# Kernel tuning notes

Hardware: AMD Instinct MI355X
Metric: run time of the kernel (lower is better)

The kernel has to match this reference:

```python
import jax, jax.numpy as jnp
import numpy as np

N_E = 1024
E_DIM = 256
BETA = 0.25
EPS = 1e-10


def setup_inputs() -> dict:
    key = jax.random.key(0)
    k1, k2 = jax.random.split(key)
    z = jax.random.normal(k1, (32, E_DIM, 32, 32), dtype=jnp.float32)
    emb = jax.random.normal(k2, (N_E, E_DIM), dtype=jnp.float32)
    return {"z": z, "emb": emb}


def reference(z, emb):
    sg = jax.lax.stop_gradient
    # (B, C, H, W) -> (B, H, W, C)
    zp = jnp.transpose(z, (0, 2, 3, 1))
    zf = zp.reshape(-1, E_DIM)  # (N, C), N = B*H*W
    # squared euclidean distances: ||z||^2 + ||e||^2 - 2 z e^T  -> (N, n_e)
    d = (jnp.sum(zf * zf, axis=1, keepdims=True)
         + jnp.sum(emb * emb, axis=1)
         - 2.0 * jnp.matmul(zf, emb.T))
    idx = jnp.argmin(d, axis=1)  # (N,)
    # one-hot @ codebook == gather (same math, no dense one-hot matmul)
    z_q1 = emb[idx].reshape(zp.shape)  # (B, H, W, C)
    # loss: note original does NOT detach z_q1 anywhere
    loss = jnp.mean((z_q1 - zp) ** 2) + BETA * jnp.mean((z_q1 - sg(zp)) ** 2)
    # straight-through (original detaches z, not z_q1)
    z_q = zp + (z_q1 - sg(zp))
    # perplexity from mean one-hot encodings = normalized histogram of indices
    counts = jnp.bincount(idx, length=N_E)
    e_mean = counts.astype(zf.dtype) / idx.shape[0]
    perplexity = jnp.exp(-jnp.sum(e_mean * jnp.log(e_mean + EPS)))
    z_q = jnp.transpose(z_q, (0, 3, 1, 2))
    z_q1_out = jnp.transpose(z_q1, (0, 3, 1, 2))
    return loss, z_q, perplexity, idx, z_q1_out
```

## Files before the change

### kernel.cpp

```cpp
#include <hip/hip_runtime.h>
#include <hip/hip_bf16.h>
#include <math.h>

#define CDIM 256
#define HW   1024
#define NVEC 32768
#define NE   1024
#define ZSIZE 8388608
#define NSPLIT 4
#define MARGIN 0.12f
#define ZPCAP 15360

#define OUT_LOSS 0
#define OUT_ZQ   1
#define OUT_PERP 8388609
#define OUT_IDX  8388610
#define OUT_ZQ1  8421378

#define WS_LOSS   0
#define WS_RCNT   64
#define WS_HIST   128
#define WS_ENORM  4224
#define WS_IDX    8448
#define WS_RLIST  139520
#define WS_S1     270592
#define WS_S2     794880
#define WS_J1     1319168
#define WS_SCORE  1843456
#define WS_EBH    2105600
#define WS_ZBH    2629888
#define WS_ZPACK  19407104

typedef __attribute__((ext_vector_type(8))) short short8;
typedef __attribute__((ext_vector_type(4))) float f32x4;
typedef __attribute__((ext_vector_type(8))) unsigned short ushort8v;
typedef __attribute__((ext_vector_type(8))) _Float16 half8;

__device__ __forceinline__ unsigned short f16_rne(float x) {
    _Float16 h = (_Float16)x;
    return __builtin_bit_cast(unsigned short, h);
}
__device__ __forceinline__ void lds_barrier() {
    asm volatile("s_waitcnt lgkmcnt(0)\n\ts_barrier" ::: "memory");
}

__global__ __launch_bounds__(256) void vq_prep(
    const float* __restrict__ z, const float* __restrict__ emb,
    unsigned short* __restrict__ zbh, unsigned short* __restrict__ ebh,
    float* __restrict__ enorm, int* __restrict__ wsz)
{
    const int tid = threadIdx.x, w = tid >> 6, L = tid & 63;
    if (blockIdx.x < 512) {
        __shared__ unsigned short th[64 * 264];
        const int b = blockIdx.x >> 4, hw0 = (blockIdx.x & 15) << 6;
        const float* zp = z + (size_t)b * (CDIM * HW) + hw0;
        for (int i = 0; i < 16; ++i) {
            int k = (i * 4 + w) * 4;
            float f0 = zp[(size_t)(k + 0) * HW + L];
            float f1 = zp[(size_t)(k + 1) * HW + L];
            float f2 = zp[(size_t)(k + 2) * HW + L];
            float f3 = zp[(size_t)(k + 3) * HW + L];
            ushort4 hi = { f16_rne(f0), f16_rne(f1), f16_rne(f2), f16_rne(f3) };
            *(ushort4*)&th[L * 264 + k] = hi;
        }
        __syncthreads();
#pragma unroll
        for (int it = 0; it < 8; ++it) {
            int row = it * 8 + (tid >> 5);
            int kc = (tid & 31) * 8;
            size_t o = (size_t)(b * 1024 + hw0 + row) * CDIM + kc;
            *(ushort8v*)(zbh + o) = *(ushort8v*)&th[row * 264 + kc];
        }
    } else {
        if (blockIdx.x == 512) {
            for (int i = tid; i < 1056; i += 256) wsz[i] = 0;
        }
        const int cb = (int)(blockIdx.x - 512) * 64;
        for (int p = 0; p < 16; ++p) {
            int code = cb + p * 4 + w;
            float4 v = *(const float4*)(emb + (size_t)code * CDIM + L * 4);
            float s = v.x * v.x + v.y * v.y + v.z * v.z + v.w * v.w;
            for (int off = 32; off; off >>= 1) s += __shfl_down(s, off, 64);
            if (L == 0) enorm[code] = s;
            ushort4 hi = { f16_rne(v.x), f16_rne(v.y), f16_rne(v.z), f16_rne(v.w) };
            *(ushort4*)(ebh + (size_t)code * CDIM + L * 4) = hi;
        }
    }
}

__global__ __launch_bounds__(256, 3) void vq_mfma3(
    const unsigned short* __restrict__ zbh, const unsigned short* __restrict__ ebh,
    const float* __restrict__ enorm,
    float* __restrict__ s1_ws, float* __restrict__ s2_ws, int* __restrict__ j1_ws)
{
    __shared__ short bbuf[2][2048];
    __shared__ float en_s[256];

    const int tid = threadIdx.x, w = tid >> 6, L = tid & 63;
    const int l15 = L & 15, q = L >> 4;
    const int r16 = tid & 15, ch = (tid >> 4) & 3;
    const int mtile = blockIdx.x & 255, js = blockIdx.x >> 8;
    const int n0 = mtile << 7;
    const int jsbase = js << 8;

    half8 AH[2][8];
#pragma unroll
    for (int mf = 0; mf < 2; ++mf)
#pragma unroll
        for (int kk = 0; kk < 8; ++kk)
            AH[mf][kk] = *(const half8*)(zbh + (size_t)(n0 + w * 32 + mf * 16 + l15) * CDIM + kk * 32 + q * 8);

    en_s[tid] = enorm[jsbase + tid];

    float s1[2][4], s2[2][4]; int j1[2][4];
#pragma unroll
    for (int mf = 0; mf < 2; ++mf)
#pragma unroll
        for (int r = 0; r < 4; ++r) { s1[mf][r] = -3.4e38f; s2[mf][r] = -3.4e38f; j1[mf][r] = 0; }

    const unsigned short* ebase = ebh + (size_t)(jsbase + w * 16 + r16) * CDIM + ch * 8;

    short8 st[2];
    st[0] = *(const short8*)(ebase);
    *(short8*)(bbuf[0] + w * 512 + L * 8) = st[0];
    st[1] = *(const short8*)(ebase + 32);
    st[0] = *(const short8*)(ebase + 64);
    lds_barrier();

    f32x4 acc[2][4];
#pragma unroll 8
    for (int t = 0; t < 32; ++t) {
        const int kk = t & 7;
        if (kk == 0) {
#pragma unroll
            for (int mf = 0; mf < 2; ++mf)
#pragma unroll
                for (int jf = 0; jf < 4; ++jf)
                    acc[mf][jf] = (f32x4){0.f, 0.f, 0.f, 0.f};
        }
        const short* bb = bbuf[t & 1];
#pragma unroll
        for (int jf = 0; jf < 4; ++jf) {
            half8 B = *(const half8*)(bb + jf * 512 + L * 8);
            acc[0][jf] = __builtin_amdgcn_mfma_f32_16x16x32_f16(AH[0][kk], B, acc[0][jf], 0, 0, 0);
            acc[1][jf] = __builtin_amdgcn_mfma_f32_16x16x32_f16(AH[1][kk], B, acc[1][jf], 0, 0, 0);
        }
        if (t < 31) {
            *(short8*)(bbuf[(t + 1) & 1] + w * 512 + L * 8) = st[(t + 1) & 1];
            if (t < 29) {
                const int t3 = t + 3;
                st[(t + 1) & 1] = *(const short8*)(ebase + (size_t)(t3 >> 3) * (64 * CDIM) + (t3 & 7) * 32);
            }
            lds_barrier();
        }
        if (kk == 7) {
            const int jg = t >> 3;
#pragma unroll
            for (int jf = 0; jf < 4; ++jf) {
                const int jl = jg * 64 + jf * 16 + l15;
                const int j = jsbase + jl;
                const float hn = 0.5f * en_s[jl];
#pragma unroll
                for (int mf = 0; mf < 2; ++mf)
#pragma unroll
                    for (int r = 0; r < 4; ++r) {
                        float s = acc[mf][jf][r] - hn;
                        if (s > s1[mf][r]) { s2[mf][r] = s1[mf][r]; s1[mf][r] = s; j1[mf][r] = j; }
                        else if (s > s2[mf][r]) s2[mf][r] = s;
                    }
            }
        }
    }

#pragma unroll
    for (int mf = 0; mf < 2; ++mf)
#pragma unroll
        for (int r = 0; r < 4; ++r) {
            float a1 = s1[mf][r], a2 = s2[mf][r]; int aj = j1[mf][r];
            for (int m = 1; m < 16; m <<= 1) {
                float o1 = __shfl_xor(a1, m, 64);
                float o2 = __shfl_xor(a2, m, 64);
                int   oj = __shfl_xor(aj, m, 64);
                if (o1 > a1 || (o1 == a1 && oj < aj)) { a2 = fmaxf(a1, o2); a1 = o1; aj = oj; }
                else a2 = fmaxf(a2, o1);
            }
            if (l15 == 0) {
                int o = js * NVEC + n0 + w * 32 + mf * 16 + q * 4 + r;
                s1_ws[o] = a1; s2_ws[o] = a2; j1_ws[o] = aj;
            }
        }
}

__global__ __launch_bounds__(256) void vq_merge(
    const float* __restrict__ s1_ws, const float* __restrict__ s2_ws,
    const int* __restrict__ j1_ws, int* __restrict__ idx_ws,
    float* __restrict__ idx_out, int* __restrict__ hist,
    int* __restrict__ rcnt, int* __restrict__ rlist,
    unsigned long long* __restrict__ score)
{
    int n = blockIdx.x * 256 + threadIdx.x;
    score[n] = 0ull;
    float b1 = -3.4e38f, b2 = -3.4e38f; int bj = 0;
#pragma unroll
    for (int s = 0; s < NSPLIT; ++s) {
        float a1 = s1_ws[s * NVEC + n], a2 = s2_ws[s * NVEC + n];
        int aj = j1_ws[s * NVEC + n];
        if (a1 > b1 || (a1 == b1 && aj < bj)) { b2 = fmaxf(b1, a2); b1 = a1; bj = aj; }
        else b2 = fmaxf(b2, a1);
    }
    if (b1 - b2 < MARGIN) {
        idx_ws[n] = -1;
        int p = atomicAdd(rcnt, 1); rlist[p] = n;
    } else {
        idx_ws[n] = bj;
        idx_out[n] = (float)bj;
        atomicAdd(&hist[bj], 1);
    }
}

__global__ __launch_bounds__(256) void vq_zpack(
    const float* __restrict__ z, const int* __restrict__ rcnt,
    const int* __restrict__ rlist, float* __restrict__ zpack)
{
    const int count = min(*rcnt, ZPCAP);
    for (int it = blockIdx.x; it < count; it += gridDim.x) {
        const int n = rlist[it];
        zpack[(size_t)it * 256 + threadIdx.x] =
            z[(size_t)(n >> 10) * (CDIM * HW) + (size_t)threadIdx.x * HW + (n & 1023)];
    }
}

__global__ __launch_bounds__(256) void vq_rescue(
    const float* __restrict__ z, const float* __restrict__ emb,
    const float* __restrict__ enorm, const int* __restrict__ rcnt,
    const int* __restrict__ rlist, const float* __restrict__ zpack,
    unsigned long long* __restrict__ score)
{
    __shared__ float en_s[64];
    __shared__ __align__(16) float zrow[256];
    __shared__ float rs[4];
    __shared__ int   rj[4];
    const int tid = threadIdx.x;
    const int wv = tid >> 6, L = tid & 63;
    const int chunk = blockIdx.x & 15;
    const int jwave = chunk * 64 + wv * 16;
    const int jodd = L >> 5;
    const int rstride = gridDim.x >> 4;
    const int count = *rcnt;

    if (tid < 64) en_s[tid] = enorm[chunk * 64 + tid];
    __syncthreads();

    for (int it = blockIdx.x >> 4; it < count; it += rstride) {
        const int n = rlist[it];
        float4 zv;
        if (it < ZPCAP) {
            zv = *(const float4*)(zpack + (size_t)it * 256 + L * 4);
        } else {
            __syncthreads();
            zrow[tid] = z[(size_t)(n >> 10) * (CDIM * HW) + (size_t)tid * HW + (n & 1023)];
            __syncthreads();
            zv = *(const float4*)&zrow[L * 4];
        }

        float b1 = -3.4e38f; int bj = 0x7fffffff;
#pragma unroll
        for (int jo = 0; jo < 16; jo += 2) {
            const int jA = jwave + jo;
            const float4 eA = *(const float4*)(emb + (size_t)jA * CDIM + L * 4);
            const float4 eB = *(const float4*)(emb + (size_t)(jA + 1) * CDIM + L * 4);
            float pA = fmaf(zv.x, eA.x, fmaf(zv.y, eA.y, fmaf(zv.z, eA.z, zv.w * eA.w)));
            float pB = fmaf(zv.x, eB.x, fmaf(zv.y, eB.y, fmaf(zv.z, eB.z, zv.w * eB.w)));
            float tA = pA + __shfl_xor(pA, 32, 64);
            float tB = pB + __shfl_xor(pB, 32, 64);
            float u = (L < 32) ? tA : tB;
            u += __shfl_xor(u, 16, 64);
            u += __shfl_xor(u, 8, 64);
            u += __shfl_xor(u, 4, 64);
            u += __shfl_xor(u, 2, 64);
            u += __shfl_xor(u, 1, 64);
            const int j = jA + jodd;
            const float s = u - 0.5f * en_s[wv * 16 + jo + jodd];
            if (s > b1) { b1 = s; bj = j; }
        }
        {
            const float o1 = __shfl_xor(b1, 32, 64);
            const int   oj = __shfl_xor(bj, 32, 64);
            if (o1 > b1 || (o1 == b1 && oj < bj)) { b1 = o1; bj = oj; }
        }
        __syncthreads();
        if (L == 0) { rs[wv] = b1; rj[wv] = bj; }
        __syncthreads();
        if (tid == 0) {
            float f1 = rs[0]; int fj = rj[0];
#pragma unroll
            for (int v = 1; v < 4; ++v)
                if (rs[v] > f1 || (rs[v] == f1 && rj[v] < fj)) { f1 = rs[v]; fj = rj[v]; }
            unsigned key = __float_as_uint(f1);
            key = (key & 0x80000000u) ? ~key : (key | 0x80000000u);
            unsigned long long packed = ((unsigned long long)key << 32) | (unsigned)(~fj);
            atomicMax(&score[n], packed);
        }
    }
}

__global__ __launch_bounds__(256) void vq_gather(
    const float* __restrict__ z, const float* __restrict__ emb,
    const int* __restrict__ idx_ws, const unsigned long long* __restrict__ score,
    float* __restrict__ zq, float* __restrict__ zq1,
    float* __restrict__ idx_out, int* __restrict__ hist,
    double* __restrict__ loss_sum)
{
    __shared__ float es[32 * 129];
    __shared__ int ids[32];
    __shared__ float wred[4];

    const int tid = threadIdx.x, w = tid >> 6, L = tid & 63;
    const int b   = blockIdx.x >> 6;
    const int half = (blockIdx.x >> 5) & 1;
    const int hw0 = (blockIdx.x & 31) << 5;
    const int n0  = (b << 10) + hw0;
    const int c0  = half << 7;

    if (tid < 32) {
        const int n = n0 + tid;
        int id = idx_ws[n];
        if (id < 0) {
            id = (int)(~(unsigned)score[n]) & (NE - 1);
            if (half == 0) {
                idx_out[n] = (float)id;
                atomicAdd(&hist[id], 1);
            }
        }
        ids[tid] = id;
    }
    __syncthreads();

#pragma unroll
    for (int p = 0; p < 4; ++p) {
        int u = p * 256 + tid;
        int r = u >> 5, cq = (u & 31) * 4;
        float4 v = *(const float4*)(emb + (size_t)ids[r] * CDIM + c0 + cq);
        es[r * 129 + cq + 0] = v.x;
        es[r * 129 + cq + 1] = v.y;
        es[r * 129 + cq + 2] = v.z;
        es[r * 129 + cq + 3] = v.w;
    }
    __syncthreads();

    const int row = L & 31, cp = L >> 5;
    const size_t zbase = (size_t)b * (CDIM * HW) + hw0 + row;
    float ls = 0.f;
    for (int rd = 0; rd < 16; ++rd) {
        int cl = rd * 8 + w * 2 + cp;
        size_t off = zbase + (size_t)(c0 + cl) * HW;
        float zv = z[off];
        float e  = es[row * 129 + cl];
        float d  = e - zv;
        zq[off]  = zv + d;
        zq1[off] = e;
        ls += d * d;
    }

    for (int off = 32; off; off >>= 1) ls += __shfl_down(ls, off, 64);
    if (L == 0) wred[w] = ls;
    __syncthreads();
    if (tid == 0)
        atomicAdd(loss_sum, (double)(wred[0] + wred[1] + wred[2] + wred[3]));
}

__global__ __launch_bounds__(1024) void vq_final(
    const int* __restrict__ hist, const double* __restrict__ loss_sum,
    float* __restrict__ out_loss, float* __restrict__ out_perp)
{
    int tid = threadIdx.x;
    float em = (float)hist[tid] * (1.0f / 32768.0f);
    float term = em * logf(em + 1e-10f);
    for (int off = 32; off; off >>= 1) term += __shfl_down(term, off, 64);
    __shared__ float red[16];
    int lane = tid & 63, wv = tid >> 6;
    if (lane == 0) red[wv] = term;
    __syncthreads();
    if (tid == 0) {
        float s = 0.f;
        for (int i = 0; i < 16; ++i) s += red[i];
        *out_perp = expf(-s);
        *out_loss = (float)(*loss_sum * 1.25 / 8388608.0);
    }
}

extern "C" void kernel_launch(void* const* d_in, const int* in_sizes, int n_in,
                              void* d_out, int out_size, void* d_ws, size_t ws_size,
                              hipStream_t stream) {
    const float* z   = (const float*)d_in[0];
    const float* emb = (const float*)d_in[1];
    float* out = (float*)d_out;
    char*  ws  = (char*)d_ws;

    double* loss_sum    = (double*)(ws + WS_LOSS);
    int*    rcnt        = (int*)(ws + WS_RCNT);
    int*    hist        = (int*)(ws + WS_HIST);
    float*  enorm       = (float*)(ws + WS_ENORM);
    int*    idx_ws      = (int*)(ws + WS_IDX);
    int*    rlist       = (int*)(ws + WS_RLIST);
    float*  s1_ws       = (float*)(ws + WS_S1);
    float*  s2_ws       = (float*)(ws + WS_S2);
    int*    j1_ws       = (int*)(ws + WS_J1);
    unsigned short* ebh = (unsigned short*)(ws + WS_EBH);
    unsigned short* zbh = (unsigned short*)(ws + WS_ZBH);
    float*  zpack       = (float*)(ws + WS_ZPACK);
    unsigned long long* score = (unsigned long long*)(ws + WS_SCORE);

    vq_prep  <<<528, 256, 0, stream>>>(z, emb, zbh, ebh, enorm, (int*)ws);
    vq_mfma3 <<<1024, 256, 0, stream>>>(zbh, ebh, enorm, s1_ws, s2_ws, j1_ws);
    vq_merge <<<128, 256, 0, stream>>>(s1_ws, s2_ws, j1_ws, idx_ws, out + OUT_IDX, hist, rcnt, rlist, score);
    vq_zpack <<<1024, 256, 0, stream>>>(z, rcnt, rlist, zpack);
    vq_rescue<<<2048, 256, 0, stream>>>(z, emb, enorm, rcnt, rlist, zpack, score);
    vq_gather<<<2048, 256, 0, stream>>>(z, emb, idx_ws, score, out + OUT_ZQ, out + OUT_ZQ1, out + OUT_IDX, hist, loss_sum);
    vq_final <<<1, 1024, 0, stream>>>(hist, loss_sum, out + OUT_LOSS, out + OUT_PERP);
}
```

Before: 233.6 us.

## Fuse merge/zpack into MFMA kernel and final reduction into gather via last-block counters

Removes the separate merge, zpack and final kernels. The last of the four split blocks for each row tile (found with an atomic counter) does the split merge, margin flagging and z packing. The last gather block computes perplexity and loss. The MFMA B-operand staging also changes from a two-slot per-k double buffer to a full 64-code panel loaded once per code group, with fewer barriers. This cuts launch overhead and intermediate kernel boundaries, at the cost of more LDS, serialized tail work in the last blocks, and fence-based inter-block ordering.

```diff
diff --git a/kernel.cpp b/kernel.cpp
--- a/kernel.cpp
+++ b/kernel.cpp
@@ -19,17 +19,20 @@
 
 #define WS_LOSS   0
 #define WS_RCNT   64
-#define WS_HIST   128
-#define WS_ENORM  4224
-#define WS_IDX    8448
-#define WS_RLIST  139520
-#define WS_S1     270592
-#define WS_S2     794880
-#define WS_J1     1319168
-#define WS_SCORE  1843456
-#define WS_EBH    2105600
-#define WS_ZBH    2629888
-#define WS_ZPACK  19407104
+#define WS_GCNT   96
+#define WS_MCNT   128
+#define WS_HIST   1152
+#define WS_ENORM  5248
+#define WS_IDX    9472
+#define WS_RLIST  140544
+#define WS_S1     271616
+#define WS_S2     795904
+#define WS_J1     1320192
+#define WS_SCORE  1844480
+#define WS_EBH    2106624
+#define WS_ZBH    2630912
+#define WS_ZPACK  19408128
+#define WS_ZERO_INTS 1312
 
 typedef __attribute__((ext_vector_type(8))) short short8;
 typedef __attribute__((ext_vector_type(4))) float f32x4;
@@ -73,7 +76,7 @@
         }
     } else {
         if (blockIdx.x == 512) {
-            for (int i = tid; i < 1056; i += 256) wsz[i] = 0;
+            for (int i = tid; i < WS_ZERO_INTS; i += 256) wsz[i] = 0;
         }
         const int cb = (int)(blockIdx.x - 512) * 64;
         for (int p = 0; p < 16; ++p) {
@@ -90,11 +93,18 @@
 
 __global__ __launch_bounds__(256, 3) void vq_mfma3(
     const unsigned short* __restrict__ zbh, const unsigned short* __restrict__ ebh,
-    const float* __restrict__ enorm,
-    float* __restrict__ s1_ws, float* __restrict__ s2_ws, int* __restrict__ j1_ws)
+    const float* __restrict__ enorm, const float* __restrict__ z,
+    float* __restrict__ s1_ws, float* __restrict__ s2_ws, int* __restrict__ j1_ws,
+    int* __restrict__ idx_ws, float* __restrict__ idx_out, int* __restrict__ hist,
+    int* __restrict__ rcnt, int* __restrict__ rlist,
+    unsigned long long* __restrict__ score, int* __restrict__ mcnt,
+    float* __restrict__ zpack)
 {
-    __shared__ short bbuf[2][2048];
+    __shared__ short bpan[32 * 512];
     __shared__ float en_s[256];
+    __shared__ int sh_flagn[128];
+    __shared__ int sh_flagp[128];
+    __shared__ int sh_fcnt, sh_last;
 
     const int tid = threadIdx.x, w = tid >> 6, L = tid & 63;
     const int l15 = L & 15, q = L >> 4;
@@ -112,71 +122,66 @@
 
     en_s[tid] = enorm[jsbase + tid];
 
-    float s1[2][4], s2[2][4]; int j1[2][4];
+    float s1[2][4], s2[2][4]; int j1v[2][4];
 #pragma unroll
     for (int mf = 0; mf < 2; ++mf)
 #pragma unroll
-        for (int r = 0; r < 4; ++r) { s1[mf][r] = -3.4e38f; s2[mf][r] = -3.4e38f; j1[mf][r] = 0; }
+        for (int r = 0; r < 4; ++r) { s1[mf][r] = -3.4e38f; s2[mf][r] = -3.4e38f; j1v[mf][r] = 0; }
 
     const unsigned short* ebase = ebh + (size_t)(jsbase + w * 16 + r16) * CDIM + ch * 8;
 
-    short8 st[2];
-    st[0] = *(const short8*)(ebase);
-    *(short8*)(bbuf[0] + w * 512 + L * 8) = st[0];
-    st[1] = *(const short8*)(ebase + 32);
-    st[0] = *(const short8*)(ebase + 64);
+    short8 st[8];
+#pragma unroll
+    for (int kk = 0; kk < 8; ++kk) st[kk] = *(const short8*)(ebase + kk * 32);
+#pragma unroll
+    for (int kk = 0; kk < 8; ++kk) *(short8*)(bpan + (w * 8 + kk) * 512 + L * 8) = st[kk];
+#pragma unroll
+    for (int kk = 0; kk < 8; ++kk) st[kk] = *(const short8*)(ebase + 64 * CDIM + kk * 32);
     lds_barrier();
 
-    f32x4 acc[2][4];
-#pragma unroll 8
-    for (int t = 0; t < 32; ++t) {
-        const int kk = t & 7;
-        if (kk == 0) {
+    for (int p = 0; p < 4; ++p) {
+        f32x4 acc[2][4] = {};
+#pragma unroll
+        for (int kk = 0; kk < 8; ++kk) {
+#pragma unroll
+            for (int jf = 0; jf < 4; ++jf) {
+                half8 B = *(const half8*)(bpan + (jf * 8 + kk) * 512 + L * 8);
+                acc[0][jf] = __builtin_amdgcn_mfma_f32_16x16x32_f16(AH[0][kk], B, acc[0][jf], 0, 0, 0);
+                acc[1][jf] = __builtin_amdgcn_mfma_f32_16x16x32_f16(AH[1][kk], B, acc[1][jf], 0, 0, 0);
+            }
+        }
+#pragma unroll
+        for (int jf = 0; jf < 4; ++jf) {
+            const int jl = p * 64 + jf * 16 + l15;
+            const int j = jsbase + jl;
+            const float hn = 0.5f * en_s[jl];
 #pragma unroll
             for (int mf = 0; mf < 2; ++mf)
 #pragma unroll
-                for (int jf = 0; jf < 4; ++jf)
-                    acc[mf][jf] = (f32x4){0.f, 0.f, 0.f, 0.f};
-        }
-        const short* bb = bbuf[t & 1];
-#pragma unroll
-        for (int jf = 0; jf < 4; ++jf) {
-            half8 B = *(const half8*)(bb + jf * 512 + L * 8);
-            acc[0][jf] = __builtin_amdgcn_mfma_f32_16x16x32_f16(AH[0][kk], B, acc[0][jf], 0, 0, 0);
-            acc[1][jf] = __builtin_amdgcn_mfma_f32_16x16x32_f16(AH[1][kk], B, acc[1][jf], 0, 0, 0);
-        }
-        if (t < 31) {
-            *(short8*)(bbuf[(t + 1) & 1] + w * 512 + L * 8) = st[(t + 1) & 1];
-            if (t < 29) {
-                const int t3 = t + 3;
-                st[(t + 1) & 1] = *(const short8*)(ebase + (size_t)(t3 >> 3) * (64 * CDIM) + (t3 & 7) * 32);
+                for (int r = 0; r < 4; ++r) {
+                    float s = acc[mf][jf][r] - hn;
+                    if (s > s1[mf][r]) { s2[mf][r] = s1[mf][r]; s1[mf][r] = s; j1v[mf][r] = j; }
+                    else if (s > s2[mf][r]) s2[mf][r] = s;
+                }
+        }
+        if (p < 3) {
+            lds_barrier();
+#pragma unroll
+            for (int kk = 0; kk < 8; ++kk) *(short8*)(bpan + (w * 8 + kk) * 512 + L * 8) = st[kk];
+            if (p < 2) {
+#pragma unroll
+                for (int kk = 0; kk < 8; ++kk)
+                    st[kk] = *(const short8*)(ebase + (size_t)(p + 2) * 64 * CDIM + kk * 32);
             }
             lds_barrier();
         }
-        if (kk == 7) {
-            const int jg = t >> 3;
-#pragma unroll
-            for (int jf = 0; jf < 4; ++jf) {
-                const int jl = jg * 64 + jf * 16 + l15;
-                const int j = jsbase + jl;
-                const float hn = 0.5f * en_s[jl];
-#pragma unroll
-                for (int mf = 0; mf < 2; ++mf)
-#pragma unroll
-                    for (int r = 0; r < 4; ++r) {
-                        float s = acc[mf][jf][r] - hn;
-                        if (s > s1[mf][r]) { s2[mf][r] = s1[mf][r]; s1[mf][r] = s; j1[mf][r] = j; }
-                        else if (s > s2[mf][r]) s2[mf][r] = s;
-                    }
-            }
-        }
     }
 
 #pragma unroll
     for (int mf = 0; mf < 2; ++mf)
 #pragma unroll
         for (int r = 0; r < 4; ++r) {
-            float a1 = s1[mf][r], a2 = s2[mf][r]; int aj = j1[mf][r];
+            float a1 = s1[mf][r], a2 = s2[mf][r]; int aj = j1v[mf][r];
             for (int m = 1; m < 16; m <<= 1) {
                 float o1 = __shfl_xor(a1, m, 64);
                 float o2 = __shfl_xor(a2, m, 64);
@@ -189,44 +194,44 @@
                 s1_ws[o] = a1; s2_ws[o] = a2; j1_ws[o] = aj;
             }
         }
-}
-
-__global__ __launch_bounds__(256) void vq_merge(
-    const float* __restrict__ s1_ws, const float* __restrict__ s2_ws,
-    const int* __restrict__ j1_ws, int* __restrict__ idx_ws,
-    float* __restrict__ idx_out, int* __restrict__ hist,
-    int* __restrict__ rcnt, int* __restrict__ rlist,
-    unsigned long long* __restrict__ score)
-{
-    int n = blockIdx.x * 256 + threadIdx.x;
-    score[n] = 0ull;
-    float b1 = -3.4e38f, b2 = -3.4e38f; int bj = 0;
-#pragma unroll
-    for (int s = 0; s < NSPLIT; ++s) {
-        float a1 = s1_ws[s * NVEC + n], a2 = s2_ws[s * NVEC + n];
-        int aj = j1_ws[s * NVEC + n];
-        if (a1 > b1 || (a1 == b1 && aj < bj)) { b2 = fmaxf(b1, a2); b1 = a1; bj = aj; }
-        else b2 = fmaxf(b2, a1);
-    }
-    if (b1 - b2 < MARGIN) {
-        idx_ws[n] = -1;
-        int p = atomicAdd(rcnt, 1); rlist[p] = n;
-    } else {
-        idx_ws[n] = bj;
-        idx_out[n] = (float)bj;
-        atomicAdd(&hist[bj], 1);
-    }
-}
-
-__global__ __launch_bounds__(256) void vq_zpack(
-    const float* __restrict__ z, const int* __restrict__ rcnt,
-    const int* __restrict__ rlist, float* __restrict__ zpack)
-{
-    const int count = min(*rcnt, ZPCAP);
-    for (int it = blockIdx.x; it < count; it += gridDim.x) {
-        const int n = rlist[it];
-        zpack[(size_t)it * 256 + threadIdx.x] =
-            z[(size_t)(n >> 10) * (CDIM * HW) + (size_t)threadIdx.x * HW + (n & 1023)];
+
+    if (tid == 0) sh_fcnt = 0;
+    __syncthreads();
+    if (tid == 0) {
+        __threadfence();
+        sh_last = (atomicAdd(&mcnt[mtile], 1) == NSPLIT - 1);
+    }
+    __syncthreads();
+    if (!sh_last) return;
+
+    if (tid < 128) {
+        const int n = n0 + tid;
+        float b1 = -3.4e38f, b2 = -3.4e38f; int bj = 0;
+#pragma unroll
+        for (int s = 0; s < NSPLIT; ++s) {
+            float a1 = s1_ws[s * NVEC + n], a2 = s2_ws[s * NVEC + n];
+            int aj = j1_ws[s * NVEC + n];
+            if (a1 > b1 || (a1 == b1 && aj < bj)) { b2 = fmaxf(b1, a2); b1 = a1; bj = aj; }
+            else b2 = fmaxf(b2, a1);
+        }
+        score[n] = 0ull;
+        if (b1 - b2 < MARGIN) {
+            idx_ws[n] = -1;
+            int pos = atomicAdd(rcnt, 1); rlist[pos] = n;
+            int c = atomicAdd(&sh_fcnt, 1); sh_flagn[c] = n; sh_flagp[c] = pos;
+        } else {
+            idx_ws[n] = bj;
+            idx_out[n] = (float)bj;
+            atomicAdd(&hist[bj], 1);
+        }
+    }
+    __syncthreads();
+    const int fc = sh_fcnt;
+    for (int i = 0; i < fc; ++i) {
+        const int n = sh_flagn[i], pos = sh_flagp[i];
+        if (pos < ZPCAP)
+            zpack[(size_t)pos * 256 + tid] =
+                z[(size_t)(n >> 10) * (CDIM * HW) + (size_t)tid * HW + (n & 1023)];
     }
 }
 
@@ -309,11 +314,13 @@
     const int* __restrict__ idx_ws, const unsigned long long* __restrict__ score,
     float* __restrict__ zq, float* __restrict__ zq1,
     float* __restrict__ idx_out, int* __restrict__ hist,
-    double* __restrict__ loss_sum)
+    double* __restrict__ loss_sum, int* __restrict__ gcnt,
+    float* __restrict__ out_loss, float* __restrict__ out_perp)
 {
     __shared__ float es[32 * 129];
     __shared__ int ids[32];
     __shared__ float wred[4];
+    __shared__ int sh_last;
 
     const int tid = threadIdx.x, w = tid >> 6, L = tid & 63;
     const int b   = blockIdx.x >> 6;
@@ -367,25 +374,27 @@
     __syncthreads();
     if (tid == 0)
         atomicAdd(loss_sum, (double)(wred[0] + wred[1] + wred[2] + wred[3]));
-}
-
-__global__ __launch_bounds__(1024) void vq_final(
-    const int* __restrict__ hist, const double* __restrict__ loss_sum,
-    float* __restrict__ out_loss, float* __restrict__ out_perp)
-{
-    int tid = threadIdx.x;
-    float em = (float)hist[tid] * (1.0f / 32768.0f);
-    float term = em * logf(em + 1e-10f);
+
+    __syncthreads();
+    if (tid == 0) {
+        __threadfence();
+        sh_last = (atomicAdd(gcnt, 1) == (int)gridDim.x - 1);
+    }
+    __syncthreads();
+    if (!sh_last) return;
+
+    float term = 0.f;
+    for (int i = tid; i < NE; i += 256) {
+        float em = (float)atomicAdd(&hist[i], 0) * (1.0f / 32768.0f);
+        term += em * logf(em + 1e-10f);
+    }
     for (int off = 32; off; off >>= 1) term += __shfl_down(term, off, 64);
-    __shared__ float red[16];
-    int lane = tid & 63, wv = tid >> 6;
-    if (lane == 0) red[wv] = term;
+    if (L == 0) wred[w] = term;
     __syncthreads();
     if (tid == 0) {
-        float s = 0.f;
-        for (int i = 0; i < 16; ++i) s += red[i];
-        *out_perp = expf(-s);
-        *out_loss = (float)(*loss_sum * 1.25 / 8388608.0);
+        double lsum = atomicAdd(loss_sum, 0.0);
+        *out_perp = expf(-(wred[0] + wred[1] + wred[2] + wred[3]));
+        *out_loss = (float)(lsum * 1.25 / 8388608.0);
     }
 }
 
@@ -399,6 +408,8 @@
 
     double* loss_sum    = (double*)(ws + WS_LOSS);
     int*    rcnt        = (int*)(ws + WS_RCNT);
+    int*    gcnt        = (int*)(ws + WS_GCNT);
+    int*    mcnt        = (int*)(ws + WS_MCNT);
     int*    hist        = (int*)(ws + WS_HIST);
     float*  enorm       = (float*)(ws + WS_ENORM);
     int*    idx_ws      = (int*)(ws + WS_IDX);
@@ -412,10 +423,11 @@
     unsigned long long* score = (unsigned long long*)(ws + WS_SCORE);
 
     vq_prep  <<<528, 256, 0, stream>>>(z, emb, zbh, ebh, enorm, (int*)ws);
-    vq_mfma3 <<<1024, 256, 0, stream>>>(zbh, ebh, enorm, s1_ws, s2_ws, j1_ws);
-    vq_merge <<<128, 256, 0, stream>>>(s1_ws, s2_ws, j1_ws, idx_ws, out + OUT_IDX, hist, rcnt, rlist, score);
-    vq_zpack <<<1024, 256, 0, stream>>>(z, rcnt, rlist, zpack);
+    vq_mfma3 <<<1024, 256, 0, stream>>>(zbh, ebh, enorm, z, s1_ws, s2_ws, j1_ws,
+                                        idx_ws, out + OUT_IDX, hist, rcnt, rlist,
+                                        score, mcnt, zpack);
     vq_rescue<<<2048, 256, 0, stream>>>(z, emb, enorm, rcnt, rlist, zpack, score);
-    vq_gather<<<2048, 256, 0, stream>>>(z, emb, idx_ws, score, out + OUT_ZQ, out + OUT_ZQ1, out + OUT_IDX, hist, loss_sum);
-    vq_final <<<1, 1024, 0, stream>>>(hist, loss_sum, out + OUT_LOSS, out + OUT_PERP);
-}
+    vq_gather<<<2048, 256, 0, stream>>>(z, emb, idx_ws, score, out + OUT_ZQ, out + OUT_ZQ1,
+                                        out + OUT_IDX, hist, loss_sum, gcnt,
+                                        out + OUT_LOSS, out + OUT_PERP);
+}
```

New measurement: 369.0 us. 1.58x slower.
